# Kernel optimization log

Measured on AMD Instinct MI355X. Metric: run time of the kernel, lower is better.

Reference implementation:

```python
import jax, jax.numpy as jnp
import numpy as np

THETA = 10000.0


def apply_rope(x, positions, theta=THETA):
    # x: [B, H, N, D], positions: [1, N] or [B, N]
    D = x.shape[-1]
    inv_freq = 1.0 / (theta ** (jnp.arange(0, D, 2, dtype=jnp.float32) / D))  # [D/2]
    ang = positions.astype(jnp.float32)[:, None, :, None] * inv_freq  # [B_or_1, 1, N, D/2]
    cos, sin = jnp.cos(ang), jnp.sin(ang)
    x1 = x[..., 0::2]
    x2 = x[..., 1::2]
    r1 = x1 * cos - x2 * sin
    r2 = x1 * sin + x2 * cos
    # interleave back to [..., D]
    return jnp.stack([r1, r2], axis=-1).reshape(x.shape)


def setup_inputs() -> dict:
    key = jax.random.key(0)
    ks = jax.random.split(key, 5)
    B, N, d_model = 2, 2048, 1024
    s = 1.0 / np.sqrt(d_model)
    return {
        "x": jax.random.normal(ks[0], (B, N, d_model), dtype=jnp.float32),
        "Wq": jax.random.normal(ks[1], (d_model, d_model), dtype=jnp.float32) * s,
        "Wk": jax.random.normal(ks[2], (d_model, d_model), dtype=jnp.float32) * s,
        "Wv": jax.random.normal(ks[3], (d_model, d_model), dtype=jnp.float32) * s,
        "Wo": jax.random.normal(ks[4], (d_model, d_model), dtype=jnp.float32) * s,
        "token_positions": jnp.arange(N, dtype=jnp.int32)[None, :],
    }


def reference(x, Wq, Wk, Wv, Wo, token_positions):
    B, N, d_model = x.shape
    H = 16
    D = d_model // H
    # projections: out = x @ W.T  (einsum '... i, j i -> ... j')
    def proj(W):
        y = jnp.einsum('bni,ji->bnj', x, W)
        return y.reshape(B, N, H, D).transpose(0, 2, 1, 3)  # [B,H,N,D]
    q, k, v = proj(Wq), proj(Wk), proj(Wv)
    q = apply_rope(q, token_positions)
    k = apply_rope(k, token_positions)
    scale = 1.0 / jnp.sqrt(jnp.asarray(D, dtype=x.dtype))
    scores = jnp.einsum('bhid,bhjd->bhij', q, k) * scale  # [B,H,N,N]
    causal = jnp.tril(jnp.ones((N, N), dtype=bool))
    scores = jnp.where(causal[None, None], scores, -jnp.inf)
    w = jax.nn.softmax(scores, axis=-1)
    o = jnp.einsum('bhij,bhjd->bhid', w, v)  # [B,H,N,D]
    o = o.transpose(0, 2, 1, 3).reshape(B, N, d_model)
    return jnp.einsum('bni,ji->bnj', o, Wo)
```

## Files before the change

kernel.cpp:

```cpp
#include <hip/hip_runtime.h>

#define DMODEL 1024
#define NSEQ   2048
#define BSZ    2
#define NH     16
#define HD     64
#define MROWS  (BSZ*NSEQ)

using short8 = __attribute__((ext_vector_type(8))) short;
using f32x4  = __attribute__((ext_vector_type(4))) float;

__device__ __forceinline__ short f2b(float f) {
  unsigned u = __builtin_bit_cast(unsigned, f);
  u += 0x7fffu + ((u >> 16) & 1u);
  return (short)(u >> 16);
}

__device__ __forceinline__ void load_lds16(const void* g, void* l) {
  __builtin_amdgcn_global_load_lds((const __attribute__((address_space(1))) unsigned int*)g,
                                   (__attribute__((address_space(3))) unsigned int*)l,
                                   16, 0, 0);
}

__global__ void cvt_all(const float* __restrict__ x,  const float* __restrict__ Wq,
                        const float* __restrict__ Wk, const float* __restrict__ Wv,
                        const float* __restrict__ Wo, const int* __restrict__ pos,
                        short* __restrict__ xb,  short* __restrict__ wqb,
                        short* __restrict__ wkb, short* __restrict__ wvb,
                        short* __restrict__ wob, float* __restrict__ cs) {
  const int NX  = (BSZ * NSEQ * DMODEL) / 4;
  const int NW  = (DMODEL * DMODEL) / 4;
  const int NCV = NX + 4 * NW;
  const int TOT = NCV + NSEQ * 32;
  for (int i = blockIdx.x * blockDim.x + threadIdx.x; i < TOT; i += gridDim.x * blockDim.x) {
    if (i < NCV) {
      const float* src; short* dst; int off;
      if (i < NX) { src = x; dst = xb; off = i; }
      else {
        int j = i - NX; int s = j >> 18; off = j & (NW - 1);
        src = (s == 0) ? Wq : (s == 1) ? Wk : (s == 2) ? Wv : Wo;
        dst = (s == 0) ? wqb : (s == 1) ? wkb : (s == 2) ? wvb : wob;
      }
      float4 v = reinterpret_cast<const float4*>(src)[off];
      short4 r;
      r.x = f2b(v.x); r.y = f2b(v.y); r.z = f2b(v.z); r.w = f2b(v.w);
      reinterpret_cast<short4*>(dst)[off] = r;
    } else {
      int idx = i - NCV;
      int n = idx >> 5, p = idx & 31;
      float inv = powf(10000.0f, -(float)(2 * p) / 64.0f);
      float ang = (float)pos[n] * inv;
      cs[idx * 2]     = cosf(ang);
      cs[idx * 2 + 1] = sinf(ang);
    }
  }
}

__global__ __launch_bounds__(512, 1) void gemm_qkv3(
    const short* __restrict__ xb,
    const short* __restrict__ wq, const short* __restrict__ wk, const short* __restrict__ wv,
    const float* __restrict__ cs,
    short* __restrict__ qb, short* __restrict__ kb, short* __restrict__ vt) {
  __shared__ short Al[2][128 * 64];
  __shared__ short Bl[2][3][128 * 64];

  const int t   = threadIdx.x;
  const int l   = t & 63;
  const int wid = t >> 6;
  const int wr  = (wid >> 2) * 64;
  const int wc  = (wid & 3) * 32;

  const int id = blockIdx.x;
  const int bx = id & 31;
  const int np = id >> 5;
  const int arow0 = bx * 128;
  const int bcol0 = np * 128;

  const int tr = t >> 3;
  const int c8 = (t & 7) ^ ((t >> 3) & 7);
  const short* W3[3] = {wq, wk, wv};

  auto STAGE = [&](int kt, int buf) {
#pragma unroll
    for (int h = 0; h < 2; ++h)
      load_lds16(xb + (size_t)(arow0 + h * 64 + tr) * DMODEL + kt * 64 + c8 * 8,
                 &Al[buf][h * 4096 + wid * 512]);
#pragma unroll
    for (int p = 0; p < 3; ++p)
#pragma unroll
      for (int h = 0; h < 2; ++h)
        load_lds16(W3[p] + (size_t)(bcol0 + h * 64 + tr) * DMODEL + kt * 64 + c8 * 8,
                   &Bl[buf][p][h * 4096 + wid * 512]);
  };

  f32x4 acc[3][4][2];
#pragma unroll
  for (int p = 0; p < 3; ++p)
#pragma unroll
    for (int mi = 0; mi < 4; ++mi)
#pragma unroll
      for (int ni = 0; ni < 2; ++ni) acc[p][mi][ni] = f32x4{0.f, 0.f, 0.f, 0.f};

  const int lr  = l & 15;
  const int lcb = (l >> 4) << 4;

  STAGE(0, 0);
  int cur = 0;

  for (int kt = 0; kt < DMODEL / 64; ++kt) {
    if (kt + 1 < DMODEL / 64) {
      STAGE(kt + 1, cur ^ 1);
      asm volatile("s_waitcnt vmcnt(8)" ::: "memory");
    } else {
      asm volatile("s_waitcnt vmcnt(0)" ::: "memory");
    }
    asm volatile("s_barrier" ::: "memory");

    const char* Ab = reinterpret_cast<const char*>(&Al[cur][0]);
#pragma unroll
    for (int ks = 0; ks < 2; ++ks) {
      const int cb = ks * 64 + lcb;
      short8 af[4];
#pragma unroll
      for (int mi = 0; mi < 4; ++mi) {
        int r = wr + mi * 16 + lr;
        af[mi] = *reinterpret_cast<const short8*>(Ab + r * 128 + (cb ^ ((r & 7) << 4)));
      }
#pragma unroll
      for (int p = 0; p < 3; ++p) {
        const char* Bb = reinterpret_cast<const char*>(&Bl[cur][p][0]);
        short8 bf[2];
#pragma unroll
        for (int ni = 0; ni < 2; ++ni) {
          int r = wc + ni * 16 + lr;
          bf[ni] = *reinterpret_cast<const short8*>(Bb + r * 128 + (cb ^ ((r & 7) << 4)));
        }
#pragma unroll
        for (int mi = 0; mi < 4; ++mi)
#pragma unroll
          for (int ni = 0; ni < 2; ++ni)
            acc[p][mi][ni] = __builtin_amdgcn_mfma_f32_16x16x32_bf16(af[mi], bf[ni], acc[p][mi][ni], 0, 0, 0);
      }
    }
    asm volatile("s_barrier" ::: "memory");
    cur ^= 1;
  }

#pragma unroll
  for (int p = 0; p < 3; ++p) {
#pragma unroll
    for (int mi = 0; mi < 4; ++mi) {
#pragma unroll
      for (int ni = 0; ni < 2; ++ni) {
#pragma unroll
        for (int r = 0; r < 4; ++r) {
          float v = acc[p][mi][ni][r];
          int m = arow0 + wr + mi * 16 + ((l >> 4) << 2) + r;
          int j = bcol0 + wc + ni * 16 + (l & 15);
          int n = m & (NSEQ - 1);
          int b = m >> 11;
          int h = j >> 6, d = j & 63, pp = d >> 1;
          float pv = __shfl_xor(v, 1);
          if (p < 2) {
            float c = cs[(n * 32 + pp) * 2];
            float s = cs[(n * 32 + pp) * 2 + 1];
            float res = (d & 1) ? (pv * s + v * c) : (v * c - pv * s);
            if (p == 0) res *= 0.180336880f;
            short* dst = (p == 0) ? qb : kb;
            dst[(((size_t)(b * NH + h)) * NSEQ + n) * HD + d] = f2b(res);
          } else {
            vt[(((size_t)(b * NH + h)) * HD + d) * NSEQ + n] = f2b(v);
          }
        }
      }
    }
  }
}

__global__ __launch_bounds__(256, 2) void gemm_out(
    const short* __restrict__ ob, const short* __restrict__ wo, float* __restrict__ out) {
  __shared__ short As[2 * 64 * 64];
  __shared__ short Bs[2 * 128 * 64];
  const int t = threadIdx.x;
  const int l = t & 63;
  const int w4 = t >> 6;
  const int wrow = (w4 >> 1) * 32;
  const int wcol = (w4 & 1) * 64;
  const int id = blockIdx.x;
  const int arow0 = (id & 63) * 64;
  const int bcol0 = (id >> 6) * 128;

  const int tr = t >> 3;
  const int c8 = (t & 7) ^ (tr & 7);

  auto STAGE = [&](int kt, int buf) {
#pragma unroll
    for (int is = 0; is < 2; ++is)
      load_lds16(ob + (size_t)(arow0 + tr + is * 32) * DMODEL + kt * 64 + c8 * 8,
                 &As[buf * 4096 + is * 2048 + (t >> 6) * 512]);
#pragma unroll
    for (int is = 0; is < 4; ++is)
      load_lds16(wo + (size_t)(bcol0 + tr + is * 32) * DMODEL + kt * 64 + c8 * 8,
                 &Bs[buf * 8192 + is * 2048 + (t >> 6) * 512]);
  };

  f32x4 acc[2][4];
#pragma unroll
  for (int mi = 0; mi < 2; ++mi)
#pragma unroll
    for (int ni = 0; ni < 4; ++ni) acc[mi][ni] = f32x4{0.f, 0.f, 0.f, 0.f};

  const int lr  = l & 15;
  const int lcb = (l >> 4) << 4;
  const int irow = (l >> 4) << 2;

  STAGE(0, 0);
  int cur = 0;

  for (int kt = 0; kt < DMODEL / 64; ++kt) {
    if (kt + 1 < DMODEL / 64) {
      STAGE(kt + 1, cur ^ 1);
      asm volatile("s_waitcnt vmcnt(6)" ::: "memory");
    } else {
      asm volatile("s_waitcnt vmcnt(0)" ::: "memory");
    }
    asm volatile("s_barrier" ::: "memory");

    const char* Ab = reinterpret_cast<const char*>(&As[cur * 4096]);
    const char* Bb = reinterpret_cast<const char*>(&Bs[cur * 8192]);
#pragma unroll
    for (int ks = 0; ks < 2; ++ks) {
      const int cb = ks * 64 + lcb;
      short8 af[2], bf[4];
#pragma unroll
      for (int mi = 0; mi < 2; ++mi) {
        int r = wrow + mi * 16 + lr;
        af[mi] = *reinterpret_cast<const short8*>(Ab + r * 128 + (cb ^ ((r & 7) << 4)));
      }
#pragma unroll
      for (int ni = 0; ni < 4; ++ni) {
        int r = wcol + ni * 16 + lr;
        bf[ni] = *reinterpret_cast<const short8*>(Bb + r * 128 + (cb ^ ((r & 7) << 4)));
      }
#pragma unroll
      for (int mi = 0; mi < 2; ++mi)
#pragma unroll
        for (int ni = 0; ni < 4; ++ni)
          acc[mi][ni] = __builtin_amdgcn_mfma_f32_16x16x32_bf16(af[mi], bf[ni], acc[mi][ni], 0, 0, 0);
    }
    asm volatile("s_barrier" ::: "memory");
    cur ^= 1;
  }

#pragma unroll
  for (int mi = 0; mi < 2; ++mi) {
#pragma unroll
    for (int ni = 0; ni < 4; ++ni) {
#pragma unroll
      for (int r = 0; r < 4; ++r) {
        int m = arow0 + wrow + mi * 16 + irow + r;
        int j = bcol0 + wcol + ni * 16 + (l & 15);
        out[(size_t)m * DMODEL + j] = acc[mi][ni][r];
      }
    }
  }
}

__global__ __launch_bounds__(512, 1) void attn(
    const short* __restrict__ qb, const short* __restrict__ kb,
    const short* __restrict__ vt, short* __restrict__ ob) {
  __shared__ short Ks[2][128 * 64];
  __shared__ short Vs[2][64 * 128];
  __shared__ short Ps[8][32 * 64];
  const int t = threadIdx.x;
  const int l = t & 63;
  const int w = t >> 6;
  const int qs = w & 3;
  const int g  = w >> 2;
  const int id  = blockIdx.x;
  const int xcd = id & 7;
  const int bh  = xcd + 8 * (id >> 6);
  const int qy  = (id >> 3) & 7;
  const short* Q  = qb + (size_t)bh * NSEQ * HD;
  const short* Kg = kb + (size_t)bh * NSEQ * HD;
  const short* Vg = vt + (size_t)bh * HD * NSEQ;
  const int b = bh >> 4, h = bh & 15;

  const int trk = t >> 3;
  const int ck  = (t & 7) ^ ((t >> 3) & 7);
  const int trv = t >> 4;
  const int cv  = (t & 15) ^ ((t >> 4) & 15);
  const int irow = (l >> 4) << 2;
  const short8 ones = {(short)0x3F80, (short)0x3F80, (short)0x3F80, (short)0x3F80,
                       (short)0x3F80, (short)0x3F80, (short)0x3F80, (short)0x3F80};

  auto STAGEA = [&](int tile, int buf) {
    int j0 = tile * 128;
#pragma unroll
    for (int is = 0; is < 2; ++is) {
      load_lds16(Kg + (size_t)(j0 + trk + is * 64) * HD + ck * 8,
                 &Ks[buf][is * 4096 + w * 512]);
      load_lds16(Vg + (size_t)(trv + is * 32) * NSEQ + j0 + cv * 8,
                 &Vs[buf][is * 4096 + w * 512]);
    }
  };

  int cur = 0;
  for (int pass = 0; pass < 2; ++pass) {
    const int qt = pass ? (15 - qy) : qy;
    const int q0 = qt * 128;
    const int nt = qt + 1;

    asm volatile("s_barrier" ::: "memory");
    STAGEA(0, cur);

    short8 qf[2][2];
    {
      int qr0 = q0 + qs * 32;
#pragma unroll
      for (int mi = 0; mi < 2; ++mi)
#pragma unroll
        for (int ks = 0; ks < 2; ++ks)
          qf[mi][ks] = *reinterpret_cast<const short8*>(
              Q + (size_t)(qr0 + mi * 16 + (l & 15)) * HD + ks * 32 + (l >> 4) * 8);
    }

    f32x4 ao[2][4];
#pragma unroll
    for (int mi = 0; mi < 2; ++mi)
#pragma unroll
      for (int dt = 0; dt < 4; ++dt) ao[mi][dt] = f32x4{0.f, 0.f, 0.f, 0.f};
    f32x4 accl[2] = {f32x4{0.f, 0.f, 0.f, 0.f}, f32x4{0.f, 0.f, 0.f, 0.f}};

    for (int tile = 0; tile < nt; ++tile) {
      if (tile + 1 < nt) {
        STAGEA(tile + 1, cur ^ 1);
        asm volatile("s_waitcnt vmcnt(4)" ::: "memory");
      } else {
        asm volatile("s_waitcnt vmcnt(0)" ::: "memory");
      }
      asm volatile("s_barrier" ::: "memory");

      const char* Kb = reinterpret_cast<const char*>(&Ks[cur][0]);
      const char* Vb = reinterpret_cast<const char*>(&Vs[cur][0]);

      f32x4 sc[4][2];
#pragma unroll
      for (int jt = 0; jt < 4; ++jt)
#pragma unroll
        for (int mi = 0; mi < 2; ++mi) sc[jt][mi] = f32x4{0.f, 0.f, 0.f, 0.f};
#pragma unroll
      for (int ks = 0; ks < 2; ++ks) {
        const int cb = ks * 64 + ((l >> 4) * 16);
#pragma unroll
        for (int jt = 0; jt < 4; ++jt) {
          int kr = g * 64 + jt * 16 + (l & 15);
          short8 kf = *reinterpret_cast<const short8*>(Kb + kr * 128 + (cb ^ ((kr & 7) << 4)));
#pragma unroll
          for (int mi = 0; mi < 2; ++mi)
            sc[jt][mi] = __builtin_amdgcn_mfma_f32_16x16x32_bf16(qf[mi][ks], kf, sc[jt][mi], 0, 0, 0);
        }
      }

      if (tile == nt - 1) {
        const int j0 = tile * 128 + g * 64;
#pragma unroll
        for (int jt = 0; jt < 4; ++jt)
#pragma unroll
          for (int mi = 0; mi < 2; ++mi)
#pragma unroll
            for (int r = 0; r < 4; ++r) {
              int i_g = q0 + qs * 32 + mi * 16 + irow + r;
              int j_g = j0 + jt * 16 + (l & 15);
              if (j_g > i_g) sc[jt][mi][r] = -1e30f;
            }
      }

#pragma unroll
      for (int jt = 0; jt < 4; ++jt) {
#pragma unroll
        for (int mi = 0; mi < 2; ++mi)
#pragma unroll
          for (int r = 0; r < 4; ++r) {
            float p = __builtin_amdgcn_exp2f(sc[jt][mi][r]);
            int i = mi * 16 + irow + r;
            int jj = jt * 16 + (l & 15);
            Ps[w][i * 64 + (jj ^ ((i & 7) << 3))] =
                (short)(__builtin_bit_cast(unsigned, p) >> 16);
          }
      }

#pragma unroll
      for (int ks2 = 0; ks2 < 2; ++ks2) {
        const int cb = ks2 * 64 + ((l >> 4) * 16);
#pragma unroll
        for (int mi = 0; mi < 2; ++mi) {
          int pr = mi * 16 + (l & 15);
          short8 pf = *reinterpret_cast<const short8*>(
              reinterpret_cast<const char*>(&Ps[w][0]) + pr * 128 + (cb ^ ((pr & 7) << 4)));
          accl[mi] = __builtin_amdgcn_mfma_f32_16x16x32_bf16(pf, ones, accl[mi], 0, 0, 0);
#pragma unroll
          for (int dt = 0; dt < 4; ++dt) {
            int vr = dt * 16 + (l & 15);
            short8 vf = *reinterpret_cast<const short8*>(
                Vb + vr * 256 + ((g * 128 + cb) ^ ((vr & 15) << 4)));
            ao[mi][dt] = __builtin_amdgcn_mfma_f32_16x16x32_bf16(pf, vf, ao[mi][dt], 0, 0, 0);
          }
        }
      }
      asm volatile("s_barrier" ::: "memory");
      cur ^= 1;
    }

    float* Opart = reinterpret_cast<float*>(&Ks[0][0]);
    float* Apart = reinterpret_cast<float*>(&Vs[0][0]);
    if (g == 1) {
#pragma unroll
      for (int mi = 0; mi < 2; ++mi) {
#pragma unroll
        for (int dt = 0; dt < 4; ++dt)
#pragma unroll
          for (int r = 0; r < 4; ++r)
            Opart[qs * 2048 + (mi * 16 + irow + r) * 64 + dt * 16 + (l & 15)] = ao[mi][dt][r];
        if ((l & 15) == 0)
#pragma unroll
          for (int r = 0; r < 4; ++r)
            Apart[qs * 32 + mi * 16 + irow + r] = accl[mi][r];
      }
    }
    asm volatile("s_barrier" ::: "memory");
    if (g == 0) {
#pragma unroll
      for (int mi = 0; mi < 2; ++mi) {
#pragma unroll
        for (int dt = 0; dt < 4; ++dt)
#pragma unroll
          for (int r = 0; r < 4; ++r)
            ao[mi][dt][r] += Opart[qs * 2048 + (mi * 16 + irow + r) * 64 + dt * 16 + (l & 15)];
#pragma unroll
        for (int r = 0; r < 4; ++r)
          accl[mi][r] += Apart[qs * 32 + mi * 16 + irow + r];
      }
#pragma unroll
      for (int mi = 0; mi < 2; ++mi)
#pragma unroll
        for (int dt = 0; dt < 4; ++dt)
#pragma unroll
          for (int r = 0; r < 4; ++r) {
            int n = q0 + qs * 32 + mi * 16 + irow + r;
            int col = h * 64 + dt * 16 + (l & 15);
            ob[((size_t)b * NSEQ + n) * DMODEL + col] = f2b(ao[mi][dt][r] / accl[mi][r]);
          }
    }
  }
}

extern "C" void kernel_launch(void* const* d_in, const int* in_sizes, int n_in,
                              void* d_out, int out_size, void* d_ws, size_t ws_size,
                              hipStream_t stream) {
  const float* x  = (const float*)d_in[0];
  const float* Wq = (const float*)d_in[1];
  const float* Wk = (const float*)d_in[2];
  const float* Wv = (const float*)d_in[3];
  const float* Wo = (const float*)d_in[4];
  const int*   pos = (const int*)d_in[5];
  float* out = (float*)d_out;
  char* ws = (char*)d_ws;

  short* xb  = (short*)(ws);
  short* wqb = (short*)(ws + ((size_t)8  << 20));
  short* wkb = (short*)(ws + ((size_t)10 << 20));
  short* wvb = (short*)(ws + ((size_t)12 << 20));
  short* wob = (short*)(ws + ((size_t)14 << 20));
  short* qb  = (short*)(ws + ((size_t)16 << 20));
  short* kb  = (short*)(ws + ((size_t)24 << 20));
  short* vt  = (short*)(ws + ((size_t)32 << 20));
  short* ob  = (short*)(ws + ((size_t)40 << 20));
  float* cs  = (float*)(ws + ((size_t)48 << 20));

  cvt_all<<<2048, 256, 0, stream>>>(x, Wq, Wk, Wv, Wo, pos, xb, wqb, wkb, wvb, wob, cs);
  gemm_qkv3<<<256, 512, 0, stream>>>(xb, wqb, wkb, wvb, cs, qb, kb, vt);
  attn<<<256, 512, 0, stream>>>(qb, kb, vt, ob);
  gemm_out<<<512, 256, 0, stream>>>(ob, wob, out);
}
```

Measured before the change: 100.8 us.

## Double attention block to 1024 threads with 16-row query strips per wave

Doubles the attention workgroup from 8 to 16 waves. Each wave now owns 16 query rows instead of 32, so per-wave MFMA work and register pressure are halved, and the K/V tile staging uses one load per thread instead of two. The cross-group partial-sum exchange through LDS gets an XOR column swizzle to reduce bank conflicts. This adds latency hiding and parallelism within a CU, but K/V fragments are re-read from LDS by twice as many waves and barriers now synchronize 16 waves.

```diff
diff --git a/kernel.cpp b/kernel.cpp
--- a/kernel.cpp
+++ b/kernel.cpp
@@ -266,17 +266,17 @@
   }
 }
 
-__global__ __launch_bounds__(512, 1) void attn(
+__global__ __launch_bounds__(1024, 1) void attn(
     const short* __restrict__ qb, const short* __restrict__ kb,
     const short* __restrict__ vt, short* __restrict__ ob) {
   __shared__ short Ks[2][128 * 64];
   __shared__ short Vs[2][64 * 128];
-  __shared__ short Ps[8][32 * 64];
+  __shared__ short Ps[16][16 * 64];
   const int t = threadIdx.x;
   const int l = t & 63;
   const int w = t >> 6;
-  const int qs = w & 3;
-  const int g  = w >> 2;
+  const int qs = w & 7;
+  const int g  = w >> 3;
   const int id  = blockIdx.x;
   const int xcd = id & 7;
   const int bh  = xcd + 8 * (id >> 6);
@@ -296,13 +296,8 @@
 
   auto STAGEA = [&](int tile, int buf) {
     int j0 = tile * 128;
-#pragma unroll
-    for (int is = 0; is < 2; ++is) {
-      load_lds16(Kg + (size_t)(j0 + trk + is * 64) * HD + ck * 8,
-                 &Ks[buf][is * 4096 + w * 512]);
-      load_lds16(Vg + (size_t)(trv + is * 32) * NSEQ + j0 + cv * 8,
-                 &Vs[buf][is * 4096 + w * 512]);
-    }
+    load_lds16(Kg + (size_t)(j0 + trk) * HD + ck * 8, &Ks[buf][t * 8]);
+    load_lds16(Vg + (size_t)trv * NSEQ + j0 + cv * 8, &Vs[buf][t * 8]);
   };
 
   int cur = 0;
@@ -314,28 +309,23 @@
     asm volatile("s_barrier" ::: "memory");
     STAGEA(0, cur);
 
-    short8 qf[2][2];
+    short8 qf[2];
     {
-      int qr0 = q0 + qs * 32;
-#pragma unroll
-      for (int mi = 0; mi < 2; ++mi)
-#pragma unroll
-        for (int ks = 0; ks < 2; ++ks)
-          qf[mi][ks] = *reinterpret_cast<const short8*>(
-              Q + (size_t)(qr0 + mi * 16 + (l & 15)) * HD + ks * 32 + (l >> 4) * 8);
-    }
-
-    f32x4 ao[2][4];
-#pragma unroll
-    for (int mi = 0; mi < 2; ++mi)
-#pragma unroll
-      for (int dt = 0; dt < 4; ++dt) ao[mi][dt] = f32x4{0.f, 0.f, 0.f, 0.f};
-    f32x4 accl[2] = {f32x4{0.f, 0.f, 0.f, 0.f}, f32x4{0.f, 0.f, 0.f, 0.f}};
+      int qrow = q0 + qs * 16 + (l & 15);
+#pragma unroll
+      for (int ks = 0; ks < 2; ++ks)
+        qf[ks] = *reinterpret_cast<const short8*>(Q + (size_t)qrow * HD + ks * 32 + (l >> 4) * 8);
+    }
+
+    f32x4 ao[4];
+#pragma unroll
+    for (int dt = 0; dt < 4; ++dt) ao[dt] = f32x4{0.f, 0.f, 0.f, 0.f};
+    f32x4 accl = f32x4{0.f, 0.f, 0.f, 0.f};
 
     for (int tile = 0; tile < nt; ++tile) {
       if (tile + 1 < nt) {
         STAGEA(tile + 1, cur ^ 1);
-        asm volatile("s_waitcnt vmcnt(4)" ::: "memory");
+        asm volatile("s_waitcnt vmcnt(2)" ::: "memory");
       } else {
         asm volatile("s_waitcnt vmcnt(0)" ::: "memory");
       }
@@ -344,11 +334,9 @@
       const char* Kb = reinterpret_cast<const char*>(&Ks[cur][0]);
       const char* Vb = reinterpret_cast<const char*>(&Vs[cur][0]);
 
-      f32x4 sc[4][2];
-#pragma unroll
-      for (int jt = 0; jt < 4; ++jt)
-#pragma unroll
-        for (int mi = 0; mi < 2; ++mi) sc[jt][mi] = f32x4{0.f, 0.f, 0.f, 0.f};
+      f32x4 sc[4];
+#pragma unroll
+      for (int jt = 0; jt < 4; ++jt) sc[jt] = f32x4{0.f, 0.f, 0.f, 0.f};
 #pragma unroll
       for (int ks = 0; ks < 2; ++ks) {
         const int cb = ks * 64 + ((l >> 4) * 16);
@@ -356,9 +344,7 @@
         for (int jt = 0; jt < 4; ++jt) {
           int kr = g * 64 + jt * 16 + (l & 15);
           short8 kf = *reinterpret_cast<const short8*>(Kb + kr * 128 + (cb ^ ((kr & 7) << 4)));
-#pragma unroll
-          for (int mi = 0; mi < 2; ++mi)
-            sc[jt][mi] = __builtin_amdgcn_mfma_f32_16x16x32_bf16(qf[mi][ks], kf, sc[jt][mi], 0, 0, 0);
+          sc[jt] = __builtin_amdgcn_mfma_f32_16x16x32_bf16(qf[ks], kf, sc[jt], 0, 0, 0);
         }
       }
 
@@ -367,45 +353,38 @@
 #pragma unroll
         for (int jt = 0; jt < 4; ++jt)
 #pragma unroll
-          for (int mi = 0; mi < 2; ++mi)
-#pragma unroll
-            for (int r = 0; r < 4; ++r) {
-              int i_g = q0 + qs * 32 + mi * 16 + irow + r;
-              int j_g = j0 + jt * 16 + (l & 15);
-              if (j_g > i_g) sc[jt][mi][r] = -1e30f;
-            }
+          for (int r = 0; r < 4; ++r) {
+            int i_g = q0 + qs * 16 + irow + r;
+            int j_g = j0 + jt * 16 + (l & 15);
+            if (j_g > i_g) sc[jt][r] = -1e30f;
+          }
       }
 
 #pragma unroll
       for (int jt = 0; jt < 4; ++jt) {
 #pragma unroll
-        for (int mi = 0; mi < 2; ++mi)
-#pragma unroll
-          for (int r = 0; r < 4; ++r) {
-            float p = __builtin_amdgcn_exp2f(sc[jt][mi][r]);
-            int i = mi * 16 + irow + r;
-            int jj = jt * 16 + (l & 15);
-            Ps[w][i * 64 + (jj ^ ((i & 7) << 3))] =
-                (short)(__builtin_bit_cast(unsigned, p) >> 16);
-          }
+        for (int r = 0; r < 4; ++r) {
+          float p = __builtin_amdgcn_exp2f(sc[jt][r]);
+          int i = irow + r;
+          int jj = jt * 16 + (l & 15);
+          Ps[w][i * 64 + (jj ^ ((i & 7) << 3))] =
+              (short)(__builtin_bit_cast(unsigned, p) >> 16);
+        }
       }
 
 #pragma unroll
       for (int ks2 = 0; ks2 < 2; ++ks2) {
         const int cb = ks2 * 64 + ((l >> 4) * 16);
-#pragma unroll
-        for (int mi = 0; mi < 2; ++mi) {
-          int pr = mi * 16 + (l & 15);
-          short8 pf = *reinterpret_cast<const short8*>(
-              reinterpret_cast<const char*>(&Ps[w][0]) + pr * 128 + (cb ^ ((pr & 7) << 4)));
-          accl[mi] = __builtin_amdgcn_mfma_f32_16x16x32_bf16(pf, ones, accl[mi], 0, 0, 0);
-#pragma unroll
-          for (int dt = 0; dt < 4; ++dt) {
-            int vr = dt * 16 + (l & 15);
-            short8 vf = *reinterpret_cast<const short8*>(
-                Vb + vr * 256 + ((g * 128 + cb) ^ ((vr & 15) << 4)));
-            ao[mi][dt] = __builtin_amdgcn_mfma_f32_16x16x32_bf16(pf, vf, ao[mi][dt], 0, 0, 0);
-          }
+        int pr = l & 15;
+        short8 pf = *reinterpret_cast<const short8*>(
+            reinterpret_cast<const char*>(&Ps[w][0]) + pr * 128 + (cb ^ ((pr & 7) << 4)));
+        accl = __builtin_amdgcn_mfma_f32_16x16x32_bf16(pf, ones, accl, 0, 0, 0);
+#pragma unroll
+        for (int dt = 0; dt < 4; ++dt) {
+          int vr = dt * 16 + (l & 15);
+          short8 vf = *reinterpret_cast<const short8*>(
+              Vb + vr * 256 + ((g * 128 + cb) ^ ((vr & 15) << 4)));
+          ao[dt] = __builtin_amdgcn_mfma_f32_16x16x32_bf16(pf, vf, ao[dt], 0, 0, 0);
         }
       }
       asm volatile("s_barrier" ::: "memory");
@@ -414,43 +393,36 @@
 
     float* Opart = reinterpret_cast<float*>(&Ks[0][0]);
     float* Apart = reinterpret_cast<float*>(&Vs[0][0]);
+    const int cswz = ((l >> 4) & 1) << 4;
     if (g == 1) {
 #pragma unroll
-      for (int mi = 0; mi < 2; ++mi) {
-#pragma unroll
-        for (int dt = 0; dt < 4; ++dt)
-#pragma unroll
-          for (int r = 0; r < 4; ++r)
-            Opart[qs * 2048 + (mi * 16 + irow + r) * 64 + dt * 16 + (l & 15)] = ao[mi][dt][r];
-        if ((l & 15) == 0)
-#pragma unroll
-          for (int r = 0; r < 4; ++r)
-            Apart[qs * 32 + mi * 16 + irow + r] = accl[mi][r];
-      }
+      for (int dt = 0; dt < 4; ++dt)
+#pragma unroll
+        for (int r = 0; r < 4; ++r)
+          Opart[qs * 1024 + (irow + r) * 64 + ((dt * 16 + (l & 15)) ^ cswz)] = ao[dt][r];
+      if ((l & 15) == 0)
+#pragma unroll
+        for (int r = 0; r < 4; ++r)
+          Apart[qs * 16 + irow + r] = accl[r];
     }
     asm volatile("s_barrier" ::: "memory");
     if (g == 0) {
 #pragma unroll
-      for (int mi = 0; mi < 2; ++mi) {
-#pragma unroll
-        for (int dt = 0; dt < 4; ++dt)
-#pragma unroll
-          for (int r = 0; r < 4; ++r)
-            ao[mi][dt][r] += Opart[qs * 2048 + (mi * 16 + irow + r) * 64 + dt * 16 + (l & 15)];
+      for (int dt = 0; dt < 4; ++dt)
 #pragma unroll
         for (int r = 0; r < 4; ++r)
-          accl[mi][r] += Apart[qs * 32 + mi * 16 + irow + r];
-      }
-#pragma unroll
-      for (int mi = 0; mi < 2; ++mi)
-#pragma unroll
-        for (int dt = 0; dt < 4; ++dt)
-#pragma unroll
-          for (int r = 0; r < 4; ++r) {
-            int n = q0 + qs * 32 + mi * 16 + irow + r;
-            int col = h * 64 + dt * 16 + (l & 15);
-            ob[((size_t)b * NSEQ + n) * DMODEL + col] = f2b(ao[mi][dt][r] / accl[mi][r]);
-          }
+          ao[dt][r] += Opart[qs * 1024 + (irow + r) * 64 + ((dt * 16 + (l & 15)) ^ cswz)];
+#pragma unroll
+      for (int r = 0; r < 4; ++r)
+        accl[r] += Apart[qs * 16 + irow + r];
+#pragma unroll
+      for (int dt = 0; dt < 4; ++dt)
+#pragma unroll
+        for (int r = 0; r < 4; ++r) {
+          int n = q0 + qs * 16 + irow + r;
+          int col = h * 64 + dt * 16 + (l & 15);
+          ob[((size_t)b * NSEQ + n) * DMODEL + col] = f2b(ao[dt][r] / accl[r]);
+        }
     }
   }
 }
@@ -480,6 +452,6 @@
 
   cvt_all<<<2048, 256, 0, stream>>>(x, Wq, Wk, Wv, Wo, pos, xb, wqb, wkb, wvb, wob, cs);
   gemm_qkv3<<<256, 512, 0, stream>>>(xb, wqb, wkb, wvb, cs, qb, kb, vt);
-  attn<<<256, 512, 0, stream>>>(qb, kb, vt, ob);
+  attn<<<256, 1024, 0, stream>>>(qb, kb, vt, ob);
   gemm_out<<<512, 256, 0, stream>>>(ob, wob, out);
 }
```

Result: no change. 99.00 us, median of 2 (-1.7%).
